# Performance work log

Measured on AMD Instinct MI355X. Metric: run time of the kernel, lower is better.

## Reference

```python
import jax, jax.numpy as jnp
import numpy as np

N = 4096
N_RBF = 16
N_HIDDEN = 64
CUTOFF = 5.0
R_MIN = 0.5
BOX = 40.0  # box side so ~30 neighbors fall within cutoff
ETA = 0.5 * (CUTOFF - R_MIN) / N_RBF  # 0.140625, matches RadialBasisLayer


def setup_inputs() -> dict:
    key = jax.random.key(0)
    ks = jax.random.split(key, 4)
    positions = jax.random.uniform(ks[0], (N, 3), dtype=jnp.float32) * BOX
    centers = jnp.linspace(R_MIN, CUTOFF, N_RBF, dtype=jnp.float32)  # buffer
    s1 = 1.0 / np.sqrt(N_RBF)
    s2 = 1.0 / np.sqrt(N_HIDDEN)
    W1 = jax.random.normal(ks[1], (N_RBF, N_HIDDEN), dtype=jnp.float32) * s1
    b1 = jnp.zeros((N_HIDDEN,), dtype=jnp.float32)
    W2 = jax.random.normal(ks[2], (N_HIDDEN, N_HIDDEN), dtype=jnp.float32) * s2
    b2 = jnp.zeros((N_HIDDEN,), dtype=jnp.float32)
    W3 = jax.random.normal(ks[3], (N_HIDDEN, 1), dtype=jnp.float32) * s2
    b3 = jnp.zeros((1,), dtype=jnp.float32)
    return {"positions": positions, "centers": centers,
            "W1": W1, "b1": b1, "W2": W2, "b2": b2, "W3": W3, "b3": b3}


def _features(positions, centers):
    # pairwise distances (N, N), safe sqrt for zero diagonal
    diff = positions[None, :, :] - positions[:, None, :]
    sq = jnp.sum(diff * diff, axis=-1)
    pos = sq > 0.0
    dist = jnp.where(pos, jnp.sqrt(jnp.where(pos, sq, 1.0)), 0.0)
    mask = pos & (dist < CUTOFF)  # (N, N)
    # RBF expansion with cosine smooth cutoff (vectorized over all pairs)
    x = dist / CUTOFF
    smooth = jnp.where(x < 1.0, 0.5 * (1.0 + jnp.cos(jnp.pi * x)), 0.0)
    w = jnp.where(mask, smooth, 0.0)  # fold mask into smooth weight (N, N)
    g = jnp.exp(-((dist[:, :, None] - centers) ** 2) / (2.0 * ETA * ETA))  # (N, N, n_rbf)
    feats = jnp.einsum('ijk,ij->ik', g, w)  # neighbor segment-sum -> (N, n_rbf)
    return feats


def reference(positions, centers, W1, b1, W2, b2, W3, b3):
    feats = _features(positions, centers)
    h = jax.nn.silu(feats @ W1 + b1)
    h = jax.nn.silu(h @ W2 + b2)
    atomic_e = (h @ W3 + b3)[:, 0]  # (N,)
    return jnp.sum(atomic_e)
```

## Files before the change

### kernel.cpp

```cpp
#include <hip/hip_runtime.h>
#include <math.h>

#define NATOMS   4096
#define NRBF     16
#define NHID     64
#define CUTOFF2  25.0f
#define INV_2ETA2 25.283950617283951f
#define PI_OVER_CUTOFF 0.62831853071795865f
#define CAP      96

#define NC1      8
#define NCELLS   512
#define CELLCAP  32
#define INV_CELL 0.2f

#define WS_ENERGY_OFF 0
#define WS_CNT_OFF    4096
#define WS_CELLS_OFF  5120
#define WS_NEED_BYTES ((size_t)(WS_CELLS_OFF + NCELLS * CELLCAP * 4) * 4)


__global__ __launch_bounds__(256) void bin_kernel(
    const float* __restrict__ pos,
    int* __restrict__ cnt,
    float4* __restrict__ cells)
{
    const int a = blockIdx.x * 256 + threadIdx.x;
    const float x = pos[3 * a + 0];
    const float y = pos[3 * a + 1];
    const float z = pos[3 * a + 2];
    const int cx = min((int)(x * INV_CELL), NC1 - 1);
    const int cy = min((int)(y * INV_CELL), NC1 - 1);
    const int cz = min((int)(z * INV_CELL), NC1 - 1);
    const int c  = (cz * NC1 + cy) * NC1 + cx;
    const int slot = atomicAdd(&cnt[c], 1);
    if (slot < CELLCAP) cells[c * CELLCAP + slot] = make_float4(x, y, z, 0.0f);
}

__global__ __launch_bounds__(256) void short_range_cells_kernel(
    const float* __restrict__ pos,
    const float* __restrict__ centers,
    const int* __restrict__ cnt,
    const float4* __restrict__ cells,
    const float* __restrict__ W1, const float* __restrict__ b1,
    const float* __restrict__ W2, const float* __restrict__ b2,
    const float* __restrict__ W3,
    float* __restrict__ ws)
{
    __shared__ float sdist[4][CAP];
    __shared__ float s_h1[4][NHID];

    const int tid  = threadIdx.x;
    const int lane = tid & 63;
    const int wave = tid >> 6;
    const int i    = blockIdx.x * 4 + wave;

    const float xi = pos[3 * i + 0];
    const float yi = pos[3 * i + 1];
    const float zi = pos[3 * i + 2];
    const int cxi = min((int)(xi * INV_CELL), NC1 - 1);
    const int cyi = min((int)(yi * INV_CELL), NC1 - 1);
    const int czi = min((int)(zi * INV_CELL), NC1 - 1);

    int nc = NCELLS;
    if (lane < 27) {
        const int cx = cxi + (lane % 3) - 1;
        const int cy = cyi + ((lane / 3) % 3) - 1;
        const int cz = czi + (lane / 9) - 1;
        if ((unsigned)cx < (unsigned)NC1 && (unsigned)cy < (unsigned)NC1 &&
            (unsigned)cz < (unsigned)NC1)
            nc = (cz * NC1 + cy) * NC1 + cx;
    }
    const int mycnt = min(cnt[nc], CELLCAP);

    const int half = lane >> 5;
    const int idx  = lane & 31;
    int base = 0;
#pragma unroll
    for (int t = 0; t < 14; ++t) {
        const int cl = 2 * t + half;
        const int c  = __shfl(nc,    cl, 64);
        const int cn = __shfl(mycnt, cl, 64);
        float sq = 1e30f;
        bool pass = false;
        if (idx < cn) {
            const float4 p = cells[c * CELLCAP + idx];
            const float dx = p.x - xi;
            const float dy = p.y - yi;
            const float dz = p.z - zi;
            sq = dx * dx + dy * dy + dz * dz;
            pass = (sq > 0.0f) && (sq < CUTOFF2);
        }
        const unsigned long long m = __ballot(pass);
        if (pass) {
            const int slot = base + (int)__popcll(m & ((1ull << lane) - 1ull));
            if (slot < CAP) sdist[wave][slot] = sqrtf(sq);
        }
        base += (int)__popcll(m);
    }
    const int count = min(base, CAP);

    const int   kf   = lane & 15;
    const int   eoff = lane >> 4;
    const float ck   = centers[kf];
    float acc = 0.0f;
    for (int e0 = 0; e0 < count; e0 += 4) {
        const int e = e0 + eoff;
        if (e < count) {
            const float d = sdist[wave][e];
            const float w = 0.5f * (1.0f + __cosf(d * PI_OVER_CUTOFF));
            const float t = d - ck;
            acc += w * __expf(-(t * t) * INV_2ETA2);
        }
    }
    acc += __shfl_xor(acc, 16, 64);
    acc += __shfl_xor(acc, 32, 64);

    float h = b1[lane];
#pragma unroll
    for (int k = 0; k < NRBF; ++k)
        h += __shfl(acc, k, 64) * W1[k * NHID + lane];
    h = h / (1.0f + __expf(-h));
    s_h1[wave][lane] = h;
    float h2 = b2[lane];
#pragma unroll 8
    for (int m = 0; m < NHID; ++m) h2 += s_h1[wave][m] * W2[m * NHID + lane];
    h2 = h2 / (1.0f + __expf(-h2));
    float e = h2 * W3[lane];
#pragma unroll
    for (int off = 32; off > 0; off >>= 1) e += __shfl_xor(e, off, 64);
    if (lane == 0) ws[i] = e;
}

__global__ __launch_bounds__(256) void reduce4k_kernel(
    const float* __restrict__ ws, const float* __restrict__ b3,
    float* __restrict__ out)
{
    __shared__ float s_part[4];
    const int tid  = threadIdx.x;
    const int lane = tid & 63;
    const int wave = tid >> 6;

    const float4* v4 = (const float4*)ws;
    float s = 0.0f;
#pragma unroll
    for (int k = 0; k < 4; ++k) {
        const float4 v = v4[tid + 256 * k];
        s += v.x + v.y + v.z + v.w;
    }
#pragma unroll
    for (int off = 32; off > 0; off >>= 1) s += __shfl_xor(s, off, 64);
    if (lane == 0) s_part[wave] = s;
    __syncthreads();
    if (tid == 0)
        out[0] = s_part[0] + s_part[1] + s_part[2] + s_part[3]
               + (float)NATOMS * b3[0];
}


#define CHUNK 1024

__global__ __launch_bounds__(256) void short_range_fb_kernel(
    const float* __restrict__ pos,
    const float* __restrict__ centers,
    const float* __restrict__ W1, const float* __restrict__ b1,
    const float* __restrict__ W2, const float* __restrict__ b2,
    const float* __restrict__ W3,
    float* __restrict__ ws)
{
    __shared__ float spos[3 * CHUNK];
    __shared__ float sdist[4][CAP];
    __shared__ float s_h1[4][NHID];
    __shared__ float s_part[4];

    const int tid  = threadIdx.x;
    const int lane = tid & 63;
    const int wave = tid >> 6;
    const int i    = blockIdx.x * 4 + wave;

    float* sx = spos;
    float* sy = spos + CHUNK;
    float* sz = spos + 2 * CHUNK;

    const float xi = pos[3 * i + 0];
    const float yi = pos[3 * i + 1];
    const float zi = pos[3 * i + 2];

    int base = 0;
    for (int c = 0; c < 4; ++c) {
        {
            const float4* src = (const float4*)(pos + c * (3 * CHUNK));
            const float4 v0 = src[3 * tid + 0];
            const float4 v1 = src[3 * tid + 1];
            const float4 v2 = src[3 * tid + 2];
            *(float4*)&sx[4 * tid] = make_float4(v0.x, v0.w, v1.z, v2.y);
            *(float4*)&sy[4 * tid] = make_float4(v0.y, v1.x, v1.w, v2.z);
            *(float4*)&sz[4 * tid] = make_float4(v0.z, v1.y, v2.x, v2.w);
        }
        __syncthreads();
#pragma unroll
        for (int it = 0; it < 4; ++it) {
            const int a = it * 256 + lane * 4;
            const float4 vx = *(const float4*)&sx[a];
            const float4 vy = *(const float4*)&sy[a];
            const float4 vz = *(const float4*)&sz[a];
#pragma unroll
            for (int u = 0; u < 4; ++u) {
                const float dx = ((const float*)&vx)[u] - xi;
                const float dy = ((const float*)&vy)[u] - yi;
                const float dz = ((const float*)&vz)[u] - zi;
                const float sq = dx * dx + dy * dy + dz * dz;
                const bool pass = (sq > 0.0f) && (sq < CUTOFF2);
                const unsigned long long mask = __ballot(pass);
                if (pass) {
                    const int slot = base + (int)__popcll(mask & ((1ull << lane) - 1ull));
                    if (slot < CAP) sdist[wave][slot] = sqrtf(sq);
                }
                base += (int)__popcll(mask);
            }
        }
        __syncthreads();
    }
    const int count = min(base, CAP);

    const int   kf   = lane & 15;
    const int   eoff = lane >> 4;
    const float ck   = centers[kf];
    float acc = 0.0f;
    for (int e0 = 0; e0 < count; e0 += 4) {
        const int e = e0 + eoff;
        if (e < count) {
            const float d = sdist[wave][e];
            const float w = 0.5f * (1.0f + __cosf(d * PI_OVER_CUTOFF));
            const float t = d - ck;
            acc += w * __expf(-(t * t) * INV_2ETA2);
        }
    }
    acc += __shfl_xor(acc, 16, 64);
    acc += __shfl_xor(acc, 32, 64);

    float h = b1[lane];
#pragma unroll
    for (int k = 0; k < NRBF; ++k)
        h += __shfl(acc, k, 64) * W1[k * NHID + lane];
    h = h / (1.0f + __expf(-h));
    s_h1[wave][lane] = h;
    float h2 = b2[lane];
#pragma unroll 8
    for (int m = 0; m < NHID; ++m) h2 += s_h1[wave][m] * W2[m * NHID + lane];
    h2 = h2 / (1.0f + __expf(-h2));
    float e = h2 * W3[lane];
#pragma unroll
    for (int off = 32; off > 0; off >>= 1) e += __shfl_xor(e, off, 64);
    if (lane == 0) s_part[wave] = e;
    __syncthreads();
    if (tid == 0)
        ws[blockIdx.x] = s_part[0] + s_part[1] + s_part[2] + s_part[3];
}

__global__ __launch_bounds__(256) void reduce_fb_kernel(
    const float* __restrict__ ws, const float* __restrict__ b3,
    float* __restrict__ out)
{
    __shared__ float s_part[4];
    const int tid  = threadIdx.x;
    const int lane = tid & 63;
    const int wave = tid >> 6;

    const float4 v = ((const float4*)ws)[tid];
    float s = v.x + v.y + v.z + v.w;
#pragma unroll
    for (int off = 32; off > 0; off >>= 1) s += __shfl_xor(s, off, 64);
    if (lane == 0) s_part[wave] = s;
    __syncthreads();
    if (tid == 0)
        out[0] = s_part[0] + s_part[1] + s_part[2] + s_part[3]
               + (float)NATOMS * b3[0];
}


extern "C" void kernel_launch(void* const* d_in, const int* in_sizes, int n_in,
                              void* d_out, int out_size, void* d_ws, size_t ws_size,
                              hipStream_t stream) {
    const float* pos     = (const float*)d_in[0];
    const float* centers = (const float*)d_in[1];
    const float* W1      = (const float*)d_in[2];
    const float* b1      = (const float*)d_in[3];
    const float* W2      = (const float*)d_in[4];
    const float* b2      = (const float*)d_in[5];
    const float* W3      = (const float*)d_in[6];
    const float* b3      = (const float*)d_in[7];
    float* out = (float*)d_out;
    float* ws  = (float*)d_ws;

    if (ws_size >= WS_NEED_BYTES) {
        int*    cnt   = (int*)(ws + WS_CNT_OFF);
        float4* cells = (float4*)(ws + WS_CELLS_OFF);
        hipMemsetAsync(cnt, 0, (NCELLS + 1) * sizeof(int), stream);
        hipLaunchKernelGGL(bin_kernel, dim3(NATOMS / 256), dim3(256), 0, stream,
                           pos, cnt, cells);
        hipLaunchKernelGGL(short_range_cells_kernel, dim3(NATOMS / 4), dim3(256), 0, stream,
                           pos, centers, cnt, cells, W1, b1, W2, b2, W3,
                           ws + WS_ENERGY_OFF);
        hipLaunchKernelGGL(reduce4k_kernel, dim3(1), dim3(256), 0, stream,
                           ws + WS_ENERGY_OFF, b3, out);
    } else {
        hipLaunchKernelGGL(short_range_fb_kernel, dim3(NATOMS / 4), dim3(256), 0, stream,
                           pos, centers, W1, b1, W2, b2, W3, ws);
        hipLaunchKernelGGL(reduce_fb_kernel, dim3(1), dim3(256), 0, stream,
                           ws, b3, out);
    }
}
```

Baseline: 85.75 us.

## Fuse binning into one block and fold final reduction via last-block atomic

Replaces the memset plus multi-block binning kernel with a single 1024-thread block that counts atoms per cell in shared memory and also resets the completion counter. The separate reduction kernel is removed: each block writes its partial energy, and the last block to arrive, detected through an atomic counter, sums all partials and writes the output. This cuts launches from four operations to two, trading that for a serialized single-block binning pass and an extra atomic per block.

```diff
diff --git a/kernel.cpp b/kernel.cpp
--- a/kernel.cpp
+++ b/kernel.cpp
@@ -8,47 +8,69 @@
 #define INV_2ETA2 25.283950617283951f
 #define PI_OVER_CUTOFF 0.62831853071795865f
 #define CAP      96
+#define NBLOCKS  (NATOMS / 4)
 
 #define NC1      8
 #define NCELLS   512
 #define CELLCAP  32
 #define INV_CELL 0.2f
 
-#define WS_ENERGY_OFF 0
+#define WS_PART_OFF   0
 #define WS_CNT_OFF    4096
+#define WS_DONE_OFF   5119
 #define WS_CELLS_OFF  5120
 #define WS_NEED_BYTES ((size_t)(WS_CELLS_OFF + NCELLS * CELLCAP * 4) * 4)
 
 
-__global__ __launch_bounds__(256) void bin_kernel(
+__global__ __launch_bounds__(1024) void bin1_kernel(
     const float* __restrict__ pos,
     int* __restrict__ cnt,
+    int* __restrict__ done,
     float4* __restrict__ cells)
 {
-    const int a = blockIdx.x * 256 + threadIdx.x;
-    const float x = pos[3 * a + 0];
-    const float y = pos[3 * a + 1];
-    const float z = pos[3 * a + 2];
-    const int cx = min((int)(x * INV_CELL), NC1 - 1);
-    const int cy = min((int)(y * INV_CELL), NC1 - 1);
-    const int cz = min((int)(z * INV_CELL), NC1 - 1);
-    const int c  = (cz * NC1 + cy) * NC1 + cx;
-    const int slot = atomicAdd(&cnt[c], 1);
-    if (slot < CELLCAP) cells[c * CELLCAP + slot] = make_float4(x, y, z, 0.0f);
+    __shared__ int lcnt[NCELLS + 1];
+    const int tid = threadIdx.x;
+    if (tid < NCELLS + 1) lcnt[tid] = 0;
+    __syncthreads();
+
+    const float4* src = (const float4*)pos;
+    const float4 v0 = src[3 * tid + 0];
+    const float4 v1 = src[3 * tid + 1];
+    const float4 v2 = src[3 * tid + 2];
+    const float xs[4] = {v0.x, v0.w, v1.z, v2.y};
+    const float ys[4] = {v0.y, v1.x, v1.w, v2.z};
+    const float zs[4] = {v0.z, v1.y, v2.x, v2.w};
+#pragma unroll
+    for (int u = 0; u < 4; ++u) {
+        const int cx = min((int)(xs[u] * INV_CELL), NC1 - 1);
+        const int cy = min((int)(ys[u] * INV_CELL), NC1 - 1);
+        const int cz = min((int)(zs[u] * INV_CELL), NC1 - 1);
+        const int c  = (cz * NC1 + cy) * NC1 + cx;
+        const int slot = atomicAdd(&lcnt[c], 1);
+        if (slot < CELLCAP)
+            cells[c * CELLCAP + slot] = make_float4(xs[u], ys[u], zs[u], 0.0f);
+    }
+    __syncthreads();
+    if (tid < NCELLS + 1) cnt[tid] = lcnt[tid];
+    if (tid == 0) *done = 0;
 }
 
 __global__ __launch_bounds__(256) void short_range_cells_kernel(
     const float* __restrict__ pos,
     const float* __restrict__ centers,
     const int* __restrict__ cnt,
+    int* __restrict__ done,
     const float4* __restrict__ cells,
     const float* __restrict__ W1, const float* __restrict__ b1,
     const float* __restrict__ W2, const float* __restrict__ b2,
-    const float* __restrict__ W3,
-    float* __restrict__ ws)
+    const float* __restrict__ W3, const float* __restrict__ b3,
+    float* __restrict__ ws,
+    float* __restrict__ out)
 {
     __shared__ float sdist[4][CAP];
     __shared__ float s_h1[4][NHID];
+    __shared__ float s_part[4];
+    __shared__ int   s_last;
 
     const int tid  = threadIdx.x;
     const int lane = tid & 63;
@@ -129,32 +151,32 @@
     float e = h2 * W3[lane];
 #pragma unroll
     for (int off = 32; off > 0; off >>= 1) e += __shfl_xor(e, off, 64);
-    if (lane == 0) ws[i] = e;
-}
-
-__global__ __launch_bounds__(256) void reduce4k_kernel(
-    const float* __restrict__ ws, const float* __restrict__ b3,
-    float* __restrict__ out)
-{
-    __shared__ float s_part[4];
-    const int tid  = threadIdx.x;
-    const int lane = tid & 63;
-    const int wave = tid >> 6;
-
-    const float4* v4 = (const float4*)ws;
-    float s = 0.0f;
-#pragma unroll
-    for (int k = 0; k < 4; ++k) {
-        const float4 v = v4[tid + 256 * k];
-        s += v.x + v.y + v.z + v.w;
-    }
-#pragma unroll
-    for (int off = 32; off > 0; off >>= 1) s += __shfl_xor(s, off, 64);
-    if (lane == 0) s_part[wave] = s;
-    __syncthreads();
-    if (tid == 0)
-        out[0] = s_part[0] + s_part[1] + s_part[2] + s_part[3]
-               + (float)NATOMS * b3[0];
+    if (lane == 0) s_part[wave] = e;
+    __syncthreads();
+
+    if (tid == 0) {
+        const float p = s_part[0] + s_part[1] + s_part[2] + s_part[3];
+        __hip_atomic_store(&ws[blockIdx.x], p, __ATOMIC_RELEASE,
+                           __HIP_MEMORY_SCOPE_AGENT);
+        const int old = __hip_atomic_fetch_add(done, 1, __ATOMIC_ACQ_REL,
+                                               __HIP_MEMORY_SCOPE_AGENT);
+        s_last = (old == NBLOCKS - 1);
+    }
+    __syncthreads();
+    if (s_last) {
+        float s = 0.0f;
+#pragma unroll
+        for (int k = 0; k < NBLOCKS / 256; ++k)
+            s += __hip_atomic_load(&ws[tid + 256 * k], __ATOMIC_RELAXED,
+                                   __HIP_MEMORY_SCOPE_AGENT);
+#pragma unroll
+        for (int off = 32; off > 0; off >>= 1) s += __shfl_xor(s, off, 64);
+        if (lane == 0) s_part[wave] = s;
+        __syncthreads();
+        if (tid == 0)
+            out[0] = s_part[0] + s_part[1] + s_part[2] + s_part[3]
+                   + (float)NATOMS * b3[0];
+    }
 }
 
 
@@ -295,15 +317,14 @@
 
     if (ws_size >= WS_NEED_BYTES) {
         int*    cnt   = (int*)(ws + WS_CNT_OFF);
+        int*    done  = (int*)(ws + WS_DONE_OFF);
         float4* cells = (float4*)(ws + WS_CELLS_OFF);
-        hipMemsetAsync(cnt, 0, (NCELLS + 1) * sizeof(int), stream);
-        hipLaunchKernelGGL(bin_kernel, dim3(NATOMS / 256), dim3(256), 0, stream,
-                           pos, cnt, cells);
-        hipLaunchKernelGGL(short_range_cells_kernel, dim3(NATOMS / 4), dim3(256), 0, stream,
-                           pos, centers, cnt, cells, W1, b1, W2, b2, W3,
-                           ws + WS_ENERGY_OFF);
-        hipLaunchKernelGGL(reduce4k_kernel, dim3(1), dim3(256), 0, stream,
-                           ws + WS_ENERGY_OFF, b3, out);
+        hipLaunchKernelGGL(bin1_kernel, dim3(1), dim3(1024), 0, stream,
+                           pos, cnt, done, cells);
+        hipLaunchKernelGGL(short_range_cells_kernel, dim3(NBLOCKS), dim3(256), 0, stream,
+                           pos, centers, cnt, done, cells,
+                           W1, b1, W2, b2, W3, b3,
+                           ws + WS_PART_OFF, out);
     } else {
         hipLaunchKernelGGL(short_range_fb_kernel, dim3(NATOMS / 4), dim3(256), 0, stream,
                            pos, centers, W1, b1, W2, b2, W3, ws);
```

New measurement: 102.2 us. 19.2% more time.
